# Kernel tuning notes

Measured on AMD Instinct MI355X. Metric: run time of the kernel, lower is better.

Reference implementation:

```python
import jax, jax.numpy as jnp
import numpy as np

N_NODES = 50000
N_HOPS = 4
N_EDGES = 800000
NFEAT = 512
HIDDEN = 512
NCLASS = 128
ATT_HID = 64


def setup_inputs() -> dict:
    key = jax.random.key(0)
    ks = jax.random.split(key, 12)
    s = lambda *sh: 1.0 / np.sqrt(sh[0])
    inp = {}
    inp['x'] = jax.random.normal(ks[0], (N_NODES, NFEAT), dtype=jnp.float32)
    inp['W1'] = jax.random.normal(ks[1], (NFEAT, HIDDEN), dtype=jnp.float32) * s(NFEAT)
    inp['W2'] = jax.random.normal(ks[2], (HIDDEN, NCLASS), dtype=jnp.float32) * s(HIDDEN)
    inp['b2'] = jax.random.normal(ks[3], (NCLASS,), dtype=jnp.float32) * 0.01
    inp['Wg'] = jax.random.normal(ks[4], (NCLASS, NCLASS), dtype=jnp.float32) * s(NCLASS)
    inp['Wa'] = jax.random.normal(ks[5], (2 * NCLASS, ATT_HID), dtype=jnp.float32) * s(2 * NCLASS)
    inp['ba'] = jax.random.normal(ks[6], (ATT_HID,), dtype=jnp.float32) * 0.01
    inp['va'] = jax.random.normal(ks[7], (ATT_HID,), dtype=jnp.float32) * s(ATT_HID)
    inp['adj_values'] = jax.random.uniform(ks[8], (N_HOPS, N_EDGES), dtype=jnp.float32)
    inp['adj_indices'] = jax.random.randint(ks[9], (N_HOPS, 2, N_EDGES), 0, N_NODES, dtype=jnp.int32)
    inp['idx'] = jnp.arange(N_NODES, dtype=jnp.int32)
    return inp


def reference(x, W1, W2, b2, Wg, Wa, ba, va, adj_values, adj_indices, idx):
    # x: [N, nfeat] -> relu(linear1) -> linear2 : [N, C]
    z = jax.nn.relu(x @ W1) @ W2 + b2  # [N, C]
    anchor = z[idx]                    # [Na, C]
    na = idx.shape[0]
    n_hops = adj_indices.shape[0]
    embs = [anchor]
    for h in range(n_hops):  # fixed small structural loop over hops
        rows = adj_indices[h, 0]  # destination anchor row per edge
        cols = adj_indices[h, 1]  # source node per edge
        # sparse matmul: agg[r] = sum_e v_e * z[cols_e]  (LayerConvol)
        agg = jax.ops.segment_sum(adj_values[h][:, None] * z[cols], rows, num_segments=na)
        embs.append(agg @ Wg)  # [Na, C]
    seq = jnp.stack(embs, axis=1)  # [Na, H+1, C]
    # AttenMlp: additive attention of anchor query over hop embeddings
    q = jnp.broadcast_to(anchor[:, None, :], seq.shape)       # [Na, H+1, C]
    feat = jnp.concatenate([q, seq], axis=-1)                 # [Na, H+1, 2C]
    scores = jnp.tanh(feat @ Wa + ba) @ va                    # [Na, H+1]
    alpha = jax.nn.softmax(scores, axis=1)
    out = jnp.einsum('nh,nhc->nc', alpha, seq)                # [Na, C]
    return jax.nn.log_softmax(out, axis=1)
```

## Files before the change

### kernel.cpp

```cpp
#include <hip/hip_runtime.h>

#define NA    50000
#define NFEAT 512
#define HID   512
#define NC    128
#define AH    64
#define NE    800000
#define NHOP  4
#define NBUCK 196
#define CAPB  5120

typedef __bf16 bf16x8 __attribute__((ext_vector_type(8)));
typedef float  f32x4  __attribute__((ext_vector_type(4)));

__device__ __forceinline__ unsigned short f2bf(float f){
  union { float f; unsigned u; } a; a.f = f;
  return (unsigned short)((a.u + 0x7fffu + ((a.u >> 16) & 1u)) >> 16);
}
__device__ __forceinline__ float bf2f(unsigned short h){
  union { unsigned u; float f; } a; a.u = ((unsigned)h) << 16;
  return a.f;
}
__device__ __forceinline__ float uasf(unsigned u){
  union { unsigned u; float f; } a; a.u = u;
  return a.f;
}
__device__ __forceinline__ float tanh_fast(float x){
  x = fminf(15.f, fmaxf(-15.f, x));
  float e = __expf(2.f * x);
  return (e - 1.f) / (e + 1.f);
}

__device__ __forceinline__ void g2l16(const void* g, void* l){
  __builtin_amdgcn_global_load_lds(
      (const __attribute__((address_space(1))) void*)g,
      (__attribute__((address_space(3))) void*)l, 16, 0, 0);
}

__global__ void prep_kernel(const float* __restrict__ W1, const float* __restrict__ W2,
                            const float* __restrict__ Wg, const float* __restrict__ Wa,
                            unsigned short* __restrict__ W1T, unsigned short* __restrict__ W2T,
                            unsigned short* __restrict__ WgT, unsigned short* __restrict__ WaT,
                            unsigned short* __restrict__ WfuseT, int* __restrict__ fill){
  const int b = blockIdx.x, tid = threadIdx.x;
  if (b < 1024){
    int i = b * 256 + tid;
    int n = i >> 9, k = i & 511;
    W1T[i] = f2bf(W1[(size_t)k * HID + n]);
  } else if (b < 1280){
    int i = (b - 1024) * 256 + tid;
    int n = i >> 9, k = i & 511;
    W2T[i] = f2bf(W2[(size_t)k * NC + n]);
  } else if (b < 1344){
    int i = (b - 1280) * 256 + tid;
    int n = i >> 7, k = i & 127;
    WgT[i] = f2bf(Wg[(size_t)k * NC + n]);
  } else if (b < 1408){
    int i = (b - 1344) * 256 + tid;
    int n = i >> 7, k = i & 127;
    float v = (n < 64) ? Wa[(size_t)k * AH + n] : Wa[(size_t)(128 + k) * AH + (n - 64)];
    WaT[i] = f2bf(v);
  } else if (b < 1440){
    int i = (b - 1408) * 256 + tid;
    int j = i >> 7, n = i & 127;
    float s = 0.f;
    for (int k = 0; k < 128; k++)
      s += Wa[(size_t)(128 + k) * AH + j] * Wg[(size_t)n * 128 + k];
    WfuseT[i] = f2bf(s);
  } else {
    int i = (b - 1440) * 256 + tid;
    if (i < NHOP * NBUCK) fill[i] = 0;
  }
}

template<int OP, int SWZ, int AF32>
__global__ __launch_bounds__(256) void gemm_bt(
    const void* __restrict__ Avoid, const unsigned short* __restrict__ BT,
    unsigned short* __restrict__ Cb, const float* __restrict__ bias,
    int M, int N, int K)
{
  int row0, col0;
  if (SWZ){
    const int xcd = blockIdx.x & 7, slot = blockIdx.x >> 3;
    const int r = xcd * 49 + (slot >> 2);
    if (r >= 391) return;
    row0 = r * 128; col0 = (slot & 3) * 128;
  } else {
    row0 = blockIdx.x * 128; col0 = blockIdx.y * 128;
  }
  const unsigned short* A16 = (const unsigned short*)Avoid;
  const float*          A32 = (const float*)Avoid;
  __shared__ unsigned short As[128 * 32];
  __shared__ unsigned short Bs[128 * 32];
  const int tid = threadIdx.x;
  const int wave = tid >> 6, lane = tid & 63;
  const int wr = (wave >> 1) * 64, wc = (wave & 1) * 64;
  f32x4 acc[4][4];
  #pragma unroll
  for (int m = 0; m < 4; m++)
    #pragma unroll
    for (int n = 0; n < 4; n++) acc[m][n] = (f32x4){0.f, 0.f, 0.f, 0.f};
  const int lrow = lane >> 2, lk = (lane & 3) * 8;

  for (int k0 = 0; k0 < K; k0 += 32){
    __syncthreads();
    #pragma unroll
    for (int j = 0; j < 2; j++){
      const int rb = (wave * 2 + j) * 16;
      const int ra = rb + lrow;
      int gr = row0 + ra; gr = gr < M ? gr : M - 1;
      if (AF32){
        const float* src = A32 + (size_t)gr * K + k0 + lk;
        float4 f0 = *reinterpret_cast<const float4*>(src);
        float4 f1 = *reinterpret_cast<const float4*>(src + 4);
        bf16x8 a;
        a[0] = (__bf16)f0.x; a[1] = (__bf16)f0.y; a[2] = (__bf16)f0.z; a[3] = (__bf16)f0.w;
        a[4] = (__bf16)f1.x; a[5] = (__bf16)f1.y; a[6] = (__bf16)f1.z; a[7] = (__bf16)f1.w;
        *reinterpret_cast<bf16x8*>(&As[ra * 32 + lk]) = a;
      } else {
        g2l16(A16 + (size_t)gr * K + k0 + lk, As + rb * 32);
      }
      int gc = col0 + ra; gc = gc < N ? gc : N - 1;
      g2l16(BT + (size_t)gc * K + k0 + lk, Bs + rb * 32);
    }
    __syncthreads();
    bf16x8 af[4], bfr[4];
    #pragma unroll
    for (int m = 0; m < 4; m++)
      af[m] = *reinterpret_cast<const bf16x8*>(&As[(wr + m * 16 + (lane & 15)) * 32 + (lane >> 4) * 8]);
    #pragma unroll
    for (int n = 0; n < 4; n++)
      bfr[n] = *reinterpret_cast<const bf16x8*>(&Bs[(wc + n * 16 + (lane & 15)) * 32 + (lane >> 4) * 8]);
    #pragma unroll
    for (int m = 0; m < 4; m++)
      #pragma unroll
      for (int n = 0; n < 4; n++)
        acc[m][n] = __builtin_amdgcn_mfma_f32_16x16x32_bf16(af[m], bfr[n], acc[m][n], 0, 0, 0);
  }

  const int rbase = row0 + wr + (lane >> 4) * 4;
  const int cbase = col0 + wc + (lane & 15);
  #pragma unroll
  for (int m = 0; m < 4; m++){
    #pragma unroll
    for (int n = 0; n < 4; n++){
      const int col = cbase + n * 16;
      #pragma unroll
      for (int i = 0; i < 4; i++){
        const int row = rbase + m * 16 + i;
        if (row < M && col < N){
          float v = acc[m][n][i];
          if (OP == 0){ v = v > 0.f ? v : 0.f; }
          else        { v += bias[col]; }
          Cb[(size_t)row * N + col] = f2bf(v);
        }
      }
    }
  }
}

__global__ __launch_bounds__(256) void gemm_sweep(
    const unsigned short* __restrict__ aggbf, const unsigned short* __restrict__ zbf,
    const unsigned short* __restrict__ WgT, const unsigned short* __restrict__ WfuseT,
    const unsigned short* __restrict__ WaT,
    unsigned short* __restrict__ embs, unsigned short* __restrict__ EW,
    unsigned short* __restrict__ ZWb)
{
  const int zi = blockIdx.z;
  const bool ew = (zi >= 4 && zi < 8);
  const int row0 = blockIdx.x * (ew ? 256 : 128);
  if (row0 >= NA) return;
  const unsigned short* A; const unsigned short* BT; unsigned short* Cb; int N;
  if (zi < 4)      { A = aggbf + (size_t)zi * NA * NC;       BT = WgT;    Cb = embs + (size_t)zi * NA * NC; N = 128; }
  else if (ew)     { A = aggbf + (size_t)(zi - 4) * NA * NC; BT = WfuseT; Cb = EW + (size_t)(zi - 4) * NA * AH; N = 64; }
  else             { A = zbf;                                BT = WaT;    Cb = ZWb; N = 128; }

  __shared__ unsigned short As[256 * 32];
  __shared__ unsigned short Bs[128 * 32];
  const int tid = threadIdx.x;
  const int wave = tid >> 6, lane = tid & 63;
  const int wr = ew ? wave * 64 : (wave >> 1) * 64;
  const int wc = ew ? 0 : (wave & 1) * 64;
  f32x4 acc[4][4];
  #pragma unroll
  for (int m = 0; m < 4; m++)
    #pragma unroll
    for (int n = 0; n < 4; n++) acc[m][n] = (f32x4){0.f, 0.f, 0.f, 0.f};
  const int lrow = lane >> 2, lk = (lane & 3) * 8;

  for (int k0 = 0; k0 < 128; k0 += 32){
    __syncthreads();
    if (ew){
      #pragma unroll
      for (int j = 0; j < 4; j++){
        const int rb = (wave * 4 + j) * 16;
        int gr = row0 + rb + lrow; gr = gr < NA ? gr : NA - 1;
        g2l16(A + (size_t)gr * 128 + k0 + lk, As + rb * 32);
      }
      {
        const int rb = wave * 16;
        int gc = rb + lrow; gc = gc < 64 ? gc : 63;
        g2l16(BT + (size_t)gc * 128 + k0 + lk, Bs + rb * 32);
      }
    } else {
      #pragma unroll
      for (int j = 0; j < 2; j++){
        const int rb = (wave * 2 + j) * 16;
        int gr = row0 + rb + lrow; gr = gr < NA ? gr : NA - 1;
        g2l16(A + (size_t)gr * 128 + k0 + lk, As + rb * 32);
        int gc = rb + lrow; gc = gc < N ? gc : N - 1;
        g2l16(BT + (size_t)gc * 128 + k0 + lk, Bs + rb * 32);
      }
    }
    __syncthreads();
    bf16x8 bfr[4];
    #pragma unroll
    for (int n = 0; n < 4; n++)
      bfr[n] = *reinterpret_cast<const bf16x8*>(&Bs[(wc + n * 16 + (lane & 15)) * 32 + (lane >> 4) * 8]);
    #pragma unroll
    for (int m = 0; m < 4; m++){
      bf16x8 a = *reinterpret_cast<const bf16x8*>(&As[(wr + m * 16 + (lane & 15)) * 32 + (lane >> 4) * 8]);
      #pragma unroll
      for (int n = 0; n < 4; n++)
        acc[m][n] = __builtin_amdgcn_mfma_f32_16x16x32_bf16(a, bfr[n], acc[m][n], 0, 0, 0);
    }
  }

  const int rbase = row0 + wr + (lane >> 4) * 4;
  const int cbase = wc + (lane & 15);
  #pragma unroll
  for (int m = 0; m < 4; m++){
    #pragma unroll
    for (int n = 0; n < 4; n++){
      const int col = cbase + n * 16;
      #pragma unroll
      for (int i = 0; i < 4; i++){
        const int row = rbase + m * 16 + i;
        if (row < NA && col < N)
          Cb[(size_t)row * N + col] = f2bf(acc[m][n][i]);
      }
    }
  }
}

__global__ __launch_bounds__(256) void binA_kernel(
    const int* __restrict__ adji, const float* __restrict__ adjv,
    int* __restrict__ fill, long long* __restrict__ binned)
{
  const int h = blockIdx.y, tid = threadIdx.x;
  const int e0 = blockIdx.x * 2048;
  __shared__ int lhist[NBUCK], lbase[NBUCK], lfill[NBUCK];
  for (int i = tid; i < NBUCK; i += 256){ lhist[i] = 0; lfill[i] = 0; }
  __syncthreads();
  int rr[8]; unsigned hh[8]; float vv[8];
  #pragma unroll
  for (int k = 0; k < 8; k++){
    int e = e0 + k * 256 + tid;
    bool ok = e < NE;
    int r = ok ? adji[(size_t)h * 2 * NE + e] : -1;
    int c = ok ? adji[(size_t)h * 2 * NE + NE + e] : 0;
    vv[k] = ok ? adjv[(size_t)h * NE + e] : 0.f;
    rr[k] = r;
    hh[k] = ((unsigned)(r & 255) << 17) | (unsigned)c;
    if (ok) atomicAdd(&lhist[r >> 8], 1);
  }
  __syncthreads();
  if (tid < NBUCK) lbase[tid] = atomicAdd(&fill[h * NBUCK + tid], lhist[tid]);
  __syncthreads();
  #pragma unroll
  for (int k = 0; k < 8; k++){
    if (rr[k] >= 0){
      int b = rr[k] >> 8;
      int p = lbase[b] + atomicAdd(&lfill[b], 1);
      if (p < CAPB)
        binned[((size_t)(h * NBUCK + b)) * CAPB + p] =
            ((long long)hh[k] << 32) | (unsigned)__float_as_int(vv[k]);
    }
  }
}

__global__ __launch_bounds__(1024) void bscan_kernel(const int* __restrict__ fill,
                                                     int* __restrict__ bbase, int* __restrict__ offs){
  __shared__ int tmp[1024];
  int tid = threadIdx.x;
  int v = (tid < NHOP * NBUCK) ? fill[tid] : 0;
  tmp[tid] = v; __syncthreads();
  for (int o = 1; o < 1024; o <<= 1){
    int t = (tid >= o) ? tmp[tid - o] : 0;
    __syncthreads();
    tmp[tid] += t;
    __syncthreads();
  }
  if (tid < NHOP * NBUCK) bbase[tid] = tmp[tid] - v;
  if (tid == 0) offs[NHOP * NA] = NHOP * NE;
}

__global__ __launch_bounds__(256) void binB_kernel(
    const int* __restrict__ fill, const int* __restrict__ bbase,
    const long long* __restrict__ binned,
    int* __restrict__ offs, long long* __restrict__ pvc)
{
  const int b = blockIdx.x, h = blockIdx.y, tid = threadIdx.x;
  const int hb = h * NBUCK + b;
  const int cnt = min(fill[hb], CAPB);
  const long long* src = binned + (size_t)hb * CAPB;
  const int gbase = bbase[hb];
  const int rowbase = b << 8;
  const int nrows = min(256, NA - rowbase);
  __shared__ long long sdata[CAPB];
  __shared__ int lhist[256], lpre[256], lfill2[256];
  lhist[tid] = 0; lfill2[tid] = 0;
  __syncthreads();
  for (int p = tid; p < cnt; p += 256)
    atomicAdd(&lhist[(unsigned)(src[p] >> 32) >> 17], 1);
  __syncthreads();
  int v = lhist[tid]; lpre[tid] = v; __syncthreads();
  for (int o = 1; o < 256; o <<= 1){
    int t = (tid >= o) ? lpre[tid - o] : 0;
    __syncthreads();
    lpre[tid] += t;
    __syncthreads();
  }
  int excl = lpre[tid] - v;
  if (tid < nrows) offs[h * NA + rowbase + tid] = gbase + excl;
  lpre[tid] = excl;
  __syncthreads();
  for (int p = tid; p < cnt; p += 256){
    long long rec = src[p];
    unsigned hi = (unsigned)(rec >> 32);
    int lr = hi >> 17;
    long long out = (rec & 0xffffffffLL) | ((long long)((hi & 0x1ffffu) << 6) << 32);
    int pos = lpre[lr] + atomicAdd(&lfill2[lr], 1);
    if (pos < CAPB) sdata[pos] = out;
    else            pvc[(size_t)gbase + pos] = out;
  }
  __syncthreads();
  for (int p = tid; p < cnt; p += 256)
    pvc[(size_t)gbase + p] = sdata[p];
}

#define GR 4
__global__ __launch_bounds__(256) void gather_kernel(
    const int* __restrict__ offs, const long long* __restrict__ pvc,
    const unsigned short* __restrict__ zbf, unsigned short* __restrict__ aggbf)
{
  const int h = blockIdx.y;
  const int w = threadIdx.x >> 6, lane = threadIdx.x & 63;
  const int row = blockIdx.x * GR + w;
  const int base = h * NA + row;
  const int s = offs[base], e = offs[base + 1];
  __shared__ alignas(16) long long srec[GR][64];
  const unsigned* z32 = (const unsigned*)zbf;
  const int4* sr2 = (const int4*)&srec[w][0];
  float a0 = 0.f, a1 = 0.f, b0 = 0.f, b1 = 0.f;
  for (int p0 = s; p0 < e; p0 += 64){
    long long r = 0;
    if (p0 + lane < e) r = __builtin_nontemporal_load(&pvc[p0 + lane]);
    srec[w][lane] = r;
    const int quads = (min(64, e - p0) + 3) >> 2;
    #pragma unroll 4
    for (int q = 0; q < quads; q++){
      int4 ra = sr2[2 * q], rb = sr2[2 * q + 1];
      unsigned z0 = z32[(unsigned)ra.y + lane];
      unsigned z1 = z32[(unsigned)ra.w + lane];
      unsigned z2 = z32[(unsigned)rb.y + lane];
      unsigned z3 = z32[(unsigned)rb.w + lane];
      float v0 = uasf((unsigned)ra.x), v1 = uasf((unsigned)ra.z);
      float v2 = uasf((unsigned)rb.x), v3 = uasf((unsigned)rb.z);
      a0 += v0 * uasf(z0 << 16); a1 += v0 * uasf(z0 & 0xffff0000u);
      b0 += v1 * uasf(z1 << 16); b1 += v1 * uasf(z1 & 0xffff0000u);
      a0 += v2 * uasf(z2 << 16); a1 += v2 * uasf(z2 & 0xffff0000u);
      b0 += v3 * uasf(z3 << 16); b1 += v3 * uasf(z3 & 0xffff0000u);
    }
  }
  ushort2 o; o.x = f2bf(a0 + b0); o.y = f2bf(a1 + b1);
  *reinterpret_cast<ushort2*>(aggbf + (size_t)base * NC + lane * 2) = o;
}

__global__ __launch_bounds__(256) void final_kernel(
    const unsigned short* __restrict__ zbf, const unsigned short* __restrict__ embs,
    const unsigned short* __restrict__ ZWb, const unsigned short* __restrict__ EW,
    const float* __restrict__ ba, const float* __restrict__ va,
    const int* __restrict__ idx, float* __restrict__ out)
{
  int tid = threadIdx.x, wave = tid >> 6, lane = tid & 63;
  int n = blockIdx.x * 4 + wave;
  if (n >= NA) return;
  int an = idx[n];
  float qa = bf2f(ZWb[(size_t)an * NC + lane]) + ba[lane];
  float vaj = va[lane];
  float sc[5];
  {
    float s0 = bf2f(ZWb[(size_t)an * NC + 64 + lane]);
    float t = tanh_fast(qa + s0) * vaj;
    #pragma unroll
    for (int o = 32; o; o >>= 1) t += __shfl_xor(t, o);
    sc[0] = t;
  }
  #pragma unroll
  for (int h = 1; h < 5; h++){
    float sh = bf2f(EW[((size_t)(h - 1) * NA + n) * AH + lane]);
    float t = tanh_fast(qa + sh) * vaj;
    #pragma unroll
    for (int o = 32; o; o >>= 1) t += __shfl_xor(t, o);
    sc[h] = t;
  }
  float m = sc[0];
  #pragma unroll
  for (int h = 1; h < 5; h++) m = fmaxf(m, sc[h]);
  float al[5], den = 0.f;
  #pragma unroll
  for (int h = 0; h < 5; h++){ al[h] = __expf(sc[h] - m); den += al[h]; }
  float inv = 1.f / den;
  float o0 = al[0] * bf2f(zbf[(size_t)an * NC + lane]);
  float o1 = al[0] * bf2f(zbf[(size_t)an * NC + 64 + lane]);
  #pragma unroll
  for (int h = 1; h < 5; h++){
    o0 += al[h] * bf2f(embs[((size_t)(h - 1) * NA + n) * NC + lane]);
    o1 += al[h] * bf2f(embs[((size_t)(h - 1) * NA + n) * NC + 64 + lane]);
  }
  o0 *= inv; o1 *= inv;
  float mx = fmaxf(o0, o1);
  #pragma unroll
  for (int o = 32; o; o >>= 1) mx = fmaxf(mx, __shfl_xor(mx, o));
  float se = __expf(o0 - mx) + __expf(o1 - mx);
  #pragma unroll
  for (int o = 32; o; o >>= 1) se += __shfl_xor(se, o);
  float ls = __logf(se);
  out[(size_t)n * NC + lane]      = o0 - mx - ls;
  out[(size_t)n * NC + 64 + lane] = o1 - mx - ls;
}


extern "C" void kernel_launch(void* const* d_in, const int* in_sizes, int n_in,
                              void* d_out, int out_size, void* d_ws, size_t ws_size,
                              hipStream_t stream)
{
  const float* x    = (const float*)d_in[0];
  const float* W1   = (const float*)d_in[1];
  const float* W2   = (const float*)d_in[2];
  const float* b2   = (const float*)d_in[3];
  const float* Wg   = (const float*)d_in[4];
  const float* Wa   = (const float*)d_in[5];
  const float* ba   = (const float*)d_in[6];
  const float* va   = (const float*)d_in[7];
  const float* adjv = (const float*)d_in[8];
  const int*   adji = (const int*)d_in[9];
  const int*   idx  = (const int*)d_in[10];
  float* out = (float*)d_out;
  (void)in_sizes; (void)n_in; (void)out_size; (void)ws_size;

  char* w = (char*)d_ws;
  auto alloc = [&](size_t b) -> char* { char* p = w; w += (b + 255) & ~(size_t)255; return p; };
  unsigned short* Scr1 = (unsigned short*)alloc((size_t)NA * NFEAT * 2);
  unsigned short* Hbuf = (unsigned short*)alloc((size_t)NA * HID * 2);
  unsigned short* W1T  = (unsigned short*)alloc((size_t)HID * NFEAT * 2);
  unsigned short* W2T  = (unsigned short*)alloc((size_t)NC * HID * 2);
  unsigned short* WgT  = (unsigned short*)alloc((size_t)NC * NC * 2);
  unsigned short* WaT  = (unsigned short*)alloc((size_t)NC * NC * 2);
  unsigned short* WfuseT = (unsigned short*)alloc((size_t)AH * NC * 2);
  unsigned short* zbf  = (unsigned short*)alloc((size_t)NA * NC * 2);
  unsigned short* ZWb  = (unsigned short*)alloc((size_t)NA * NC * 2);
  int* fill  = (int*)alloc((size_t)NHOP * NBUCK * 4);
  int* bbase = (int*)alloc((size_t)NHOP * NBUCK * 4);
  int* offs  = (int*)alloc(((size_t)NHOP * NA + 1) * 4);
  long long* pvc = (long long*)alloc((size_t)NHOP * NE * 8);
  long long* binned     = (long long*)Scr1;
  unsigned short* embs  = Scr1;
  unsigned short* aggbf = Hbuf;
  unsigned short* EW    = (unsigned short*)pvc;

  prep_kernel<<<dim3(1444), 256, 0, stream>>>(W1, W2, Wg, Wa, W1T, W2T, WgT, WaT, WfuseT, fill);

  gemm_bt<0, 1, 1><<<dim3(1568, 1, 1), 256, 0, stream>>>(x, W1T, Hbuf, nullptr, NA, HID, NFEAT);
  gemm_bt<1, 0, 0><<<dim3(391, 1, 1), 256, 0, stream>>>(Hbuf, W2T, zbf, b2, NA, NC, HID);

  binA_kernel<<<dim3((NE + 2047) / 2048, NHOP), 256, 0, stream>>>(adji, adjv, fill, binned);
  bscan_kernel<<<dim3(1), 1024, 0, stream>>>(fill, bbase, offs);
  binB_kernel<<<dim3(NBUCK, NHOP), 256, 0, stream>>>(fill, bbase, binned, offs, pvc);

  gather_kernel<<<dim3(NA / GR, NHOP), 256, 0, stream>>>(offs, pvc, zbf, aggbf);
  gemm_sweep<<<dim3(391, 1, 9), 256, 0, stream>>>(aggbf, zbf, WgT, WfuseT, WaT, embs, EW, ZWb);

  final_kernel<<<dim3(NA / 4), 256, 0, stream>>>(zbf, embs, ZWb, EW, ba, va, idx, out);
}
```

Measured before the change: 336.8 us.

## Reassociate Wg into the second linear layer so gather yields hop embeddings directly

Precomputes W2·Wg and b2·Wg, and widens the second GEMM to 256 output columns so it emits both z and zg = z·Wg in one pass. Because the sparse aggregation is linear, gathering zg gives the hop embeddings directly, which removes the four per-hop 128x128 GEMMs from the sweep kernel. The attention projection of the embeddings then uses Wa's second half instead of the fused Wa·Wg matrix. The cost is a wider second GEMM, an extra N×128 buffer, and different bf16 rounding order.

```diff
diff --git a/kernel.cpp b/kernel.cpp
--- a/kernel.cpp
+++ b/kernel.cpp
@@ -39,9 +39,10 @@
 
 __global__ void prep_kernel(const float* __restrict__ W1, const float* __restrict__ W2,
                             const float* __restrict__ Wg, const float* __restrict__ Wa,
-                            unsigned short* __restrict__ W1T, unsigned short* __restrict__ W2T,
-                            unsigned short* __restrict__ WgT, unsigned short* __restrict__ WaT,
-                            unsigned short* __restrict__ WfuseT, int* __restrict__ fill){
+                            const float* __restrict__ b2,
+                            unsigned short* __restrict__ W1T, unsigned short* __restrict__ W2cT,
+                            unsigned short* __restrict__ WaT, float* __restrict__ b2c,
+                            int* __restrict__ fill){
   const int b = blockIdx.x, tid = threadIdx.x;
   if (b < 1024){
     int i = b * 256 + tid;
@@ -50,46 +51,42 @@
   } else if (b < 1280){
     int i = (b - 1024) * 256 + tid;
     int n = i >> 9, k = i & 511;
-    W2T[i] = f2bf(W2[(size_t)k * NC + n]);
-  } else if (b < 1344){
+    W2cT[i] = f2bf(W2[(size_t)k * NC + n]);
+  } else if (b < 1536){
     int i = (b - 1280) * 256 + tid;
-    int n = i >> 7, k = i & 127;
-    WgT[i] = f2bf(Wg[(size_t)k * NC + n]);
-  } else if (b < 1408){
-    int i = (b - 1344) * 256 + tid;
+    int n = i >> 9, k = i & 511;
+    float s = 0.f;
+    for (int j = 0; j < 128; j++)
+      s += W2[(size_t)k * NC + j] * Wg[(size_t)j * NC + n];
+    W2cT[65536 + i] = f2bf(s);
+  } else if (b < 1600){
+    int i = (b - 1536) * 256 + tid;
     int n = i >> 7, k = i & 127;
     float v = (n < 64) ? Wa[(size_t)k * AH + n] : Wa[(size_t)(128 + k) * AH + (n - 64)];
     WaT[i] = f2bf(v);
-  } else if (b < 1440){
-    int i = (b - 1408) * 256 + tid;
-    int j = i >> 7, n = i & 127;
-    float s = 0.f;
-    for (int k = 0; k < 128; k++)
-      s += Wa[(size_t)(128 + k) * AH + j] * Wg[(size_t)n * 128 + k];
-    WfuseT[i] = f2bf(s);
+  } else if (b == 1600){
+    if (tid < 128) b2c[tid] = b2[tid];
+    else {
+      int n = tid - 128;
+      float s = 0.f;
+      for (int j = 0; j < 128; j++) s += b2[j] * Wg[(size_t)j * NC + n];
+      b2c[128 + n] = s;
+    }
   } else {
-    int i = (b - 1440) * 256 + tid;
+    int i = (b - 1601) * 256 + tid;
     if (i < NHOP * NBUCK) fill[i] = 0;
   }
 }
 
-template<int OP, int SWZ, int AF32>
-__global__ __launch_bounds__(256) void gemm_bt(
-    const void* __restrict__ Avoid, const unsigned short* __restrict__ BT,
-    unsigned short* __restrict__ Cb, const float* __restrict__ bias,
-    int M, int N, int K)
-{
-  int row0, col0;
-  if (SWZ){
-    const int xcd = blockIdx.x & 7, slot = blockIdx.x >> 3;
-    const int r = xcd * 49 + (slot >> 2);
-    if (r >= 391) return;
-    row0 = r * 128; col0 = (slot & 3) * 128;
-  } else {
-    row0 = blockIdx.x * 128; col0 = blockIdx.y * 128;
-  }
-  const unsigned short* A16 = (const unsigned short*)Avoid;
-  const float*          A32 = (const float*)Avoid;
+__global__ __launch_bounds__(256) void gemm1_kernel(
+    const float* __restrict__ A32, const unsigned short* __restrict__ BT,
+    unsigned short* __restrict__ Cb)
+{
+  const int xcd = blockIdx.x & 7, slot = blockIdx.x >> 3;
+  const int r = xcd * 49 + (slot >> 2);
+  if (r >= 391) return;
+  const int row0 = r * 128, col0 = (slot & 3) * 128;
+  const int M = NA, N = HID, K = NFEAT;
   __shared__ unsigned short As[128 * 32];
   __shared__ unsigned short Bs[128 * 32];
   const int tid = threadIdx.x;
@@ -109,17 +106,13 @@
       const int rb = (wave * 2 + j) * 16;
       const int ra = rb + lrow;
       int gr = row0 + ra; gr = gr < M ? gr : M - 1;
-      if (AF32){
-        const float* src = A32 + (size_t)gr * K + k0 + lk;
-        float4 f0 = *reinterpret_cast<const float4*>(src);
-        float4 f1 = *reinterpret_cast<const float4*>(src + 4);
-        bf16x8 a;
-        a[0] = (__bf16)f0.x; a[1] = (__bf16)f0.y; a[2] = (__bf16)f0.z; a[3] = (__bf16)f0.w;
-        a[4] = (__bf16)f1.x; a[5] = (__bf16)f1.y; a[6] = (__bf16)f1.z; a[7] = (__bf16)f1.w;
-        *reinterpret_cast<bf16x8*>(&As[ra * 32 + lk]) = a;
-      } else {
-        g2l16(A16 + (size_t)gr * K + k0 + lk, As + rb * 32);
-      }
+      const float* src = A32 + (size_t)gr * K + k0 + lk;
+      float4 f0 = *reinterpret_cast<const float4*>(src);
+      float4 f1 = *reinterpret_cast<const float4*>(src + 4);
+      bf16x8 a;
+      a[0] = (__bf16)f0.x; a[1] = (__bf16)f0.y; a[2] = (__bf16)f0.z; a[3] = (__bf16)f0.w;
+      a[4] = (__bf16)f1.x; a[5] = (__bf16)f1.y; a[6] = (__bf16)f1.z; a[7] = (__bf16)f1.w;
+      *reinterpret_cast<bf16x8*>(&As[ra * 32 + lk]) = a;
       int gc = col0 + ra; gc = gc < N ? gc : N - 1;
       g2l16(BT + (size_t)gc * K + k0 + lk, Bs + rb * 32);
     }
@@ -148,10 +141,9 @@
       #pragma unroll
       for (int i = 0; i < 4; i++){
         const int row = rbase + m * 16 + i;
-        if (row < M && col < N){
+        if (row < M){
           float v = acc[m][n][i];
-          if (OP == 0){ v = v > 0.f ? v : 0.f; }
-          else        { v += bias[col]; }
+          v = v > 0.f ? v : 0.f;
           Cb[(size_t)row * N + col] = f2bf(v);
         }
       }
@@ -159,21 +151,88 @@
   }
 }
 
+__global__ __launch_bounds__(256) void gemm2_kernel(
+    const unsigned short* __restrict__ H, const unsigned short* __restrict__ W2cT,
+    const float* __restrict__ b2c,
+    unsigned short* __restrict__ zbf, unsigned short* __restrict__ zg)
+{
+  const int xcd = blockIdx.x & 7, slot = blockIdx.x >> 3;
+  const int r = xcd * 49 + (slot >> 1);
+  if (r >= 391) return;
+  const int row0 = r * 128, col0 = (slot & 1) * 128;
+  const int K = HID;
+  __shared__ unsigned short As[128 * 32];
+  __shared__ unsigned short Bs[128 * 32];
+  const int tid = threadIdx.x;
+  const int wave = tid >> 6, lane = tid & 63;
+  const int wr = (wave >> 1) * 64, wc = (wave & 1) * 64;
+  f32x4 acc[4][4];
+  #pragma unroll
+  for (int m = 0; m < 4; m++)
+    #pragma unroll
+    for (int n = 0; n < 4; n++) acc[m][n] = (f32x4){0.f, 0.f, 0.f, 0.f};
+  const int lrow = lane >> 2, lk = (lane & 3) * 8;
+
+  for (int k0 = 0; k0 < K; k0 += 32){
+    __syncthreads();
+    #pragma unroll
+    for (int j = 0; j < 2; j++){
+      const int rb = (wave * 2 + j) * 16;
+      const int ra = rb + lrow;
+      int gr = row0 + ra; gr = gr < NA ? gr : NA - 1;
+      g2l16(H + (size_t)gr * K + k0 + lk, As + rb * 32);
+      int gc = col0 + ra;
+      g2l16(W2cT + (size_t)gc * K + k0 + lk, Bs + rb * 32);
+    }
+    __syncthreads();
+    bf16x8 af[4], bfr[4];
+    #pragma unroll
+    for (int m = 0; m < 4; m++)
+      af[m] = *reinterpret_cast<const bf16x8*>(&As[(wr + m * 16 + (lane & 15)) * 32 + (lane >> 4) * 8]);
+    #pragma unroll
+    for (int n = 0; n < 4; n++)
+      bfr[n] = *reinterpret_cast<const bf16x8*>(&Bs[(wc + n * 16 + (lane & 15)) * 32 + (lane >> 4) * 8]);
+    #pragma unroll
+    for (int m = 0; m < 4; m++)
+      #pragma unroll
+      for (int n = 0; n < 4; n++)
+        acc[m][n] = __builtin_amdgcn_mfma_f32_16x16x32_bf16(af[m], bfr[n], acc[m][n], 0, 0, 0);
+  }
+
+  const int rbase = row0 + wr + (lane >> 4) * 4;
+  const int cbase = col0 + wc + (lane & 15);
+  #pragma unroll
+  for (int m = 0; m < 4; m++){
+    #pragma unroll
+    for (int n = 0; n < 4; n++){
+      const int col = cbase + n * 16;
+      #pragma unroll
+      for (int i = 0; i < 4; i++){
+        const int row = rbase + m * 16 + i;
+        if (row < NA){
+          float v = acc[m][n][i] + b2c[col];
+          unsigned short o = f2bf(v);
+          if (col < 128) zbf[(size_t)row * NC + col] = o;
+          else           zg[(size_t)row * NC + (col - 128)] = o;
+        }
+      }
+    }
+  }
+}
+
 __global__ __launch_bounds__(256) void gemm_sweep(
-    const unsigned short* __restrict__ aggbf, const unsigned short* __restrict__ zbf,
-    const unsigned short* __restrict__ WgT, const unsigned short* __restrict__ WfuseT,
+    const unsigned short* __restrict__ embs, const unsigned short* __restrict__ zbf,
     const unsigned short* __restrict__ WaT,
-    unsigned short* __restrict__ embs, unsigned short* __restrict__ EW,
-    unsigned short* __restrict__ ZWb)
+    unsigned short* __restrict__ EW, unsigned short* __restrict__ ZWb)
 {
   const int zi = blockIdx.z;
-  const bool ew = (zi >= 4 && zi < 8);
+  const bool ew = zi < 4;
   const int row0 = blockIdx.x * (ew ? 256 : 128);
   if (row0 >= NA) return;
-  const unsigned short* A; const unsigned short* BT; unsigned short* Cb; int N;
-  if (zi < 4)      { A = aggbf + (size_t)zi * NA * NC;       BT = WgT;    Cb = embs + (size_t)zi * NA * NC; N = 128; }
-  else if (ew)     { A = aggbf + (size_t)(zi - 4) * NA * NC; BT = WfuseT; Cb = EW + (size_t)(zi - 4) * NA * AH; N = 64; }
-  else             { A = zbf;                                BT = WaT;    Cb = ZWb; N = 128; }
+  const unsigned short* A  = ew ? embs + (size_t)zi * NA * NC : zbf;
+  const unsigned short* BT = ew ? WaT + 64 * 128 : WaT;
+  unsigned short* Cb       = ew ? EW + (size_t)zi * NA * AH : ZWb;
+  const int N = ew ? 64 : 128;
 
   __shared__ unsigned short As[256 * 32];
   __shared__ unsigned short Bs[128 * 32];
@@ -342,7 +401,7 @@
 #define GR 4
 __global__ __launch_bounds__(256) void gather_kernel(
     const int* __restrict__ offs, const long long* __restrict__ pvc,
-    const unsigned short* __restrict__ zbf, unsigned short* __restrict__ aggbf)
+    const unsigned short* __restrict__ zg, unsigned short* __restrict__ embs)
 {
   const int h = blockIdx.y;
   const int w = threadIdx.x >> 6, lane = threadIdx.x & 63;
@@ -350,7 +409,7 @@
   const int base = h * NA + row;
   const int s = offs[base], e = offs[base + 1];
   __shared__ alignas(16) long long srec[GR][64];
-  const unsigned* z32 = (const unsigned*)zbf;
+  const unsigned* z32 = (const unsigned*)zg;
   const int4* sr2 = (const int4*)&srec[w][0];
   float a0 = 0.f, a1 = 0.f, b0 = 0.f, b1 = 0.f;
   for (int p0 = s; p0 < e; p0 += 64){
@@ -374,7 +433,7 @@
     }
   }
   ushort2 o; o.x = f2bf(a0 + b0); o.y = f2bf(a1 + b1);
-  *reinterpret_cast<ushort2*>(aggbf + (size_t)base * NC + lane * 2) = o;
+  *reinterpret_cast<ushort2*>(embs + (size_t)base * NC + lane * 2) = o;
 }
 
 __global__ __launch_bounds__(256) void final_kernel(
@@ -455,11 +514,11 @@
   unsigned short* Scr1 = (unsigned short*)alloc((size_t)NA * NFEAT * 2);
   unsigned short* Hbuf = (unsigned short*)alloc((size_t)NA * HID * 2);
   unsigned short* W1T  = (unsigned short*)alloc((size_t)HID * NFEAT * 2);
-  unsigned short* W2T  = (unsigned short*)alloc((size_t)NC * HID * 2);
-  unsigned short* WgT  = (unsigned short*)alloc((size_t)NC * NC * 2);
+  unsigned short* W2cT = (unsigned short*)alloc((size_t)256 * HID * 2);
   unsigned short* WaT  = (unsigned short*)alloc((size_t)NC * NC * 2);
-  unsigned short* WfuseT = (unsigned short*)alloc((size_t)AH * NC * 2);
+  float*          b2c  = (float*)alloc(256 * 4);
   unsigned short* zbf  = (unsigned short*)alloc((size_t)NA * NC * 2);
+  unsigned short* zg   = (unsigned short*)alloc((size_t)NA * NC * 2);
   unsigned short* ZWb  = (unsigned short*)alloc((size_t)NA * NC * 2);
   int* fill  = (int*)alloc((size_t)NHOP * NBUCK * 4);
   int* bbase = (int*)alloc((size_t)NHOP * NBUCK * 4);
@@ -467,20 +526,19 @@
   long long* pvc = (long long*)alloc((size_t)NHOP * NE * 8);
   long long* binned     = (long long*)Scr1;
   unsigned short* embs  = Scr1;
-  unsigned short* aggbf = Hbuf;
   unsigned short* EW    = (unsigned short*)pvc;
 
-  prep_kernel<<<dim3(1444), 256, 0, stream>>>(W1, W2, Wg, Wa, W1T, W2T, WgT, WaT, WfuseT, fill);
-
-  gemm_bt<0, 1, 1><<<dim3(1568, 1, 1), 256, 0, stream>>>(x, W1T, Hbuf, nullptr, NA, HID, NFEAT);
-  gemm_bt<1, 0, 0><<<dim3(391, 1, 1), 256, 0, stream>>>(Hbuf, W2T, zbf, b2, NA, NC, HID);
+  prep_kernel<<<dim3(1605), 256, 0, stream>>>(W1, W2, Wg, Wa, b2, W1T, W2cT, WaT, b2c, fill);
+
+  gemm1_kernel<<<dim3(1568), 256, 0, stream>>>(x, W1T, Hbuf);
+  gemm2_kernel<<<dim3(784), 256, 0, stream>>>(Hbuf, W2cT, b2c, zbf, zg);
 
   binA_kernel<<<dim3((NE + 2047) / 2048, NHOP), 256, 0, stream>>>(adji, adjv, fill, binned);
   bscan_kernel<<<dim3(1), 1024, 0, stream>>>(fill, bbase, offs);
   binB_kernel<<<dim3(NBUCK, NHOP), 256, 0, stream>>>(fill, bbase, binned, offs, pvc);
 
-  gather_kernel<<<dim3(NA / GR, NHOP), 256, 0, stream>>>(offs, pvc, zbf, aggbf);
-  gemm_sweep<<<dim3(391, 1, 9), 256, 0, stream>>>(aggbf, zbf, WgT, WfuseT, WaT, embs, EW, ZWb);
+  gather_kernel<<<dim3(NA / GR, NHOP), 256, 0, stream>>>(offs, pvc, zg, embs);
+  gemm_sweep<<<dim3(391, 1, 5), 256, 0, stream>>>(embs, zbf, WaT, EW, ZWb);
 
   final_kernel<<<dim3(NA / 4), 256, 0, stream>>>(zbf, embs, ZWb, EW, ba, va, idx, out);
 }
```

Measured after the change: 342.0 us. About the same (+1.5%).
